# Optimization experiments

Hardware: AMD Instinct MI355X
Metric: run time of the kernel (lower is better)

The kernel has to match this reference:

```python
import jax, jax.numpy as jnp
import numpy as np

N = 10000      # nodes
E = 160000     # edges
F_IN = 84
H = 256
P = 4          # powers [0,1,2,3]
L = 3          # mixhop layers


def setup_inputs() -> dict:
    key = jax.random.key(0)
    ks = jax.random.split(key, 10)
    s = 0.05
    inp = {}
    inp["x"] = jax.random.normal(ks[0], (N, F_IN), jnp.float32)
    inp["edge_index"] = jax.random.randint(ks[1], (2, E), 0, N, dtype=jnp.int32)
    inp["w_in"] = jax.random.normal(ks[2], (F_IN, H), jnp.float32) * s
    inp["b_in"] = jnp.zeros((H,), jnp.float32)
    inp["mh_w0"] = jax.random.normal(ks[3], (P, H, H), jnp.float32) * s
    inp["mh_b0"] = jnp.zeros((P, H), jnp.float32)
    inp["mh_w12"] = jax.random.normal(ks[4], (2, P, P * H, H), jnp.float32) * s
    inp["mh_b12"] = jnp.zeros((2, P, H), jnp.float32)
    inp["ln_g"] = jnp.ones((L, P * H), jnp.float32)
    inp["ln_b"] = jnp.zeros((L, P * H), jnp.float32)
    inp["w1"] = jax.random.normal(ks[5], (P * H, H), jnp.float32) * s
    inp["b1"] = jnp.zeros((H,), jnp.float32)
    inp["w2"] = jax.random.normal(ks[6], (H, H // 2), jnp.float32) * s
    inp["b2"] = jnp.zeros((H // 2,), jnp.float32)
    inp["w3"] = jax.random.normal(ks[7], (H // 2, 1), jnp.float32) * s
    inp["b3"] = jnp.zeros((1,), jnp.float32)
    return inp


def _gcn_norm(edge_index, n):
    # D^{-1/2} (A + I) D^{-1/2}, PyG gcn_norm with add_self_loops=True
    loop = jnp.arange(n, dtype=edge_index.dtype)
    src = jnp.concatenate([edge_index[0], loop])
    dst = jnp.concatenate([edge_index[1], loop])
    deg = jax.ops.segment_sum(jnp.ones(src.shape[0], jnp.float32), dst, num_segments=n)
    dinv = jnp.where(deg > 0, deg ** -0.5, 0.0)
    return src, dst, dinv[src] * dinv[dst]


def _propagate(h, src, dst, w, n):
    # out[i] = sum_{(j->i)} w_e * h[j]
    return jax.ops.segment_sum(h[src] * w[:, None], dst, num_segments=n)


def _mixhop(h, src, dst, w, n, W, B):
    outs = [h @ W[0] + B[0]]  # power 0
    for p in range(1, W.shape[0]):
        h = _propagate(h, src, dst, w, n)
        outs.append(h @ W[p] + B[p])
    return jnp.concatenate(outs, axis=-1)  # [n, P*H]


def _layernorm(x, g, b, eps=1e-5):
    mu = x.mean(-1, keepdims=True)
    var = x.var(-1, keepdims=True)
    return (x - mu) * jax.lax.rsqrt(var + eps) * g + b


def reference(x, edge_index, w_in, b_in, mh_w0, mh_b0, mh_w12, mh_b12,
              ln_g, ln_b, w1, b1, w2, b2, w3, b3):
    gelu = lambda t: jax.nn.gelu(t, approximate=False)  # torch default (erf)
    n = x.shape[0]
    src, dst, w = _gcn_norm(edge_index, n)
    h = gelu(x @ w_in + b_in)
    for i in range(L):
        W, B = (mh_w0, mh_b0) if i == 0 else (mh_w12[i - 1], mh_b12[i - 1])
        h = _mixhop(h, src, dst, w, n, W, B)
        h = gelu(_layernorm(h, ln_g[i], ln_b[i]))
        # dropout inactive at inference
    h = gelu(h @ w1 + b1)
    h = gelu(h @ w2 + b2)
    out = h @ w3 + b3
    return out.squeeze(-1)  # [N]
```

## Files before the change

### kernel.cpp

```cpp
#include <hip/hip_runtime.h>

typedef unsigned short u16;
typedef unsigned char u8;
typedef unsigned int u32;
typedef __bf16 bf16x8 __attribute__((ext_vector_type(8)));
typedef float f32x4 __attribute__((ext_vector_type(4)));
typedef float f32x2 __attribute__((ext_vector_type(2)));

#define NN 10000
#define EE 160000
#define MPAD 10112

__device__ inline float b2f(u16 u) { return __uint_as_float(((u32)u) << 16); }
__device__ inline u16 f2b(float f) {
    u32 u = __float_as_uint(f);
    return (u16)((u + 0x7fffu + ((u >> 16) & 1u)) >> 16);
}
__device__ inline u8 f2f8(float v) {
    return (u8)(__builtin_amdgcn_cvt_pk_fp8_f32(v, v, 0, false) & 0xff);
}
__device__ inline float gelu_f(float x) {
    return 0.5f * x * (1.0f + erff(x * 0.70710678118654752f));
}
__device__ inline void load_lds16(const u16* g, u16* l) {
    __builtin_amdgcn_global_load_lds((const __attribute__((address_space(1))) u32*)g,
                                     (__attribute__((address_space(3))) u32*)l, 16, 0, 0);
}

__global__ __launch_bounds__(256) void k_scan(const int* __restrict__ cnt, int* __restrict__ rowptr,
                                              int* __restrict__ cursor, float* __restrict__ dinv) {
    __shared__ int part[256];
    const int t = threadIdx.x;
    const int CH = 40;
    int base = t * CH;
    int ssum = 0;
    for (int k = 0; k < CH; k++) { int i = base + k; if (i < NN) ssum += cnt[i]; }
    part[t] = ssum;
    __syncthreads();
    for (int off = 1; off < 256; off <<= 1) {
        int v = (t >= off) ? part[t - off] : 0;
        __syncthreads();
        part[t] += v;
        __syncthreads();
    }
    int run = part[t] - ssum;
    for (int k = 0; k < CH; k++) {
        int i = base + k;
        if (i < NN) {
            rowptr[i] = run; cursor[i] = run;
            int c = cnt[i];
            dinv[i] = rsqrtf((float)(c + 1));
            run += c;
        }
    }
    if (t == 255) rowptr[NN] = run;
}

__global__ __launch_bounds__(256) void k_fill(const int* __restrict__ src, const int* __restrict__ dst,
                                              int* __restrict__ cursor, int* __restrict__ cols,
                                              float* __restrict__ vals, const float* __restrict__ dinv) {
    int e = blockIdx.x * 256 + threadIdx.x;
    if (e < EE) {
        int s = src[e], d = dst[e];
        int pos = atomicAdd(&cursor[d], 1);
        cols[pos] = s;
        vals[pos] = dinv[s] * dinv[d];
    }
}

struct TT { const float* src; u16* dst; int K, Nc, Kp; };
struct CvtSrcs { const float *b_in, *mh_b0, *mh_b12, *ln_g, *ln_b, *b1, *b2, *w3, *b3; };
__global__ __launch_bounds__(256) void k_ingest(TT t0, TT t1, TT t2, TT t3, TT t4,
                                                const float* __restrict__ x, u16* __restrict__ xp,
                                                CvtSrcs S, u16* __restrict__ smallC,
                                                const int* __restrict__ dstA, int* __restrict__ cnt) {
    int b = blockIdx.x;
    const int t = threadIdx.x;
    if (b < 656) {
        TT T;
        if (b < 8)        { T = t0; }
        else if (b < 72)  { T = t1; b -= 8; }
        else if (b < 584) { T = t2; b -= 72; }
        else if (b < 648) { T = t3; b -= 584; }
        else              { T = t4; b -= 648; }
        int tk = (T.Kp + 63) >> 6, tn = T.Nc >> 6;
        int bb  = b / (tk * tn);
        int rem = b - bb * (tk * tn);
        int k0 = (rem / tn) * 64, n0 = (rem % tn) * 64;
        __shared__ u16 tile[64][65];
        const float* src = T.src + (size_t)bb * T.K * T.Nc;
        u16* dst = T.dst + (size_t)bb * T.Nc * T.Kp;
        int c = t & 63, r0 = t >> 6;
#pragma unroll
        for (int i = 0; i < 16; i++) {
            int r = r0 + i * 4;
            int k = k0 + r;
            u16 v = 0;
            if (k < T.K) v = f2b(src[(size_t)k * T.Nc + n0 + c]);
            tile[r][c] = v;
        }
        __syncthreads();
        int rr = t & 63, cc0 = t >> 6;
#pragma unroll
        for (int i = 0; i < 16; i++) {
            int cc = cc0 + i * 4;
            int k = k0 + rr;
            if (k < T.Kp) dst[(size_t)(n0 + cc) * T.Kp + k] = tile[rr][cc];
        }
    } else if (b < 5712) {
        int idx = (b - 656) * 256 + t;
        int r = idx >> 7, c = idx & 127;
        u16 v = 0;
        if (r < NN && c < 84) v = f2b(x[(size_t)r * 84 + c]);
        xp[idx] = v;
    } else if (b < 5752) {
        int i = (b - 5712) * 256 + t;
        const float* s; int base;
        if (i < 256)       { s = S.b_in;   base = 0; }
        else if (i < 1280) { s = S.mh_b0;  base = 256; }
        else if (i < 3328) { s = S.mh_b12; base = 1280; }
        else if (i < 6400) { s = S.ln_g;   base = 3328; }
        else if (i < 9472) { s = S.ln_b;   base = 6400; }
        else if (i < 9728) { s = S.b1;     base = 9472; }
        else if (i < 9856) { s = S.b2;     base = 9728; }
        else if (i < 9984) { s = S.w3;     base = 9856; }
        else if (i < 9985) { s = S.b3;     base = 9984; }
        else return;
        smallC[i] = f2b(s[i - base]);
    } else {
        int e = (b - 5752) * 256 + t;
        if (e < EE) atomicAdd(&cnt[dstA[e]], 1);
    }
}

template<int TM, int TN, int ACT, int EPI, int BATCH>
__global__ __launch_bounds__(256) void k_gemm(const u16* __restrict__ A0, const u16* __restrict__ A1,
                                              const u16* __restrict__ A2, const u16* __restrict__ A3,
                                              const u16* __restrict__ Bt, const u16* __restrict__ bias,
                                              u16* __restrict__ C, u8* __restrict__ Z,
                                              const u16* __restrict__ w3c, const u16* __restrict__ b3c,
                                              float* __restrict__ fout,
                                              int K, int ldc, int col0, int NB_M, int NB_N) {
    constexpr int AM = TM / 32, AN = TN / 32;
    constexpr int CA = TM / 16, CB = TN / 16;
    constexpr int NCH = (CA + CB) / 4;
    constexpr int SLOT = (TM + TN) * 32;
    __shared__ __align__(16) u16 Sh[4][SLOT];
    __shared__ float shred[2][64];
    int id = blockIdx.x;
    int g8 = id & 7, sIdx = id >> 3;
    int nb = sIdx % NB_N, jb = sIdx / NB_N;
    int mb = g8 + 8 * jb;
    if (mb >= NB_M) return;
    const u16* A = A0;
    if (BATCH) {
        int z = blockIdx.y;
        if (z == 1) A = A1; else if (z == 2) A = A2; else if (z == 3) A = A3;
        Bt   += (size_t)z * 256 * K;
        bias += z * 256;
        col0 += z * 256;
    }
    const int t = threadIdx.x;
    const int wv = t >> 6, lane = t & 63;
    const int wm = wv >> 1, wn = wv & 1;
    const int quad = lane >> 4, l16 = lane & 15;
    const int tileM = mb * TM, tileN = nb * TN;

    f32x4 acc[AM][AN] = {};

    const int rch = lane >> 2, c8 = (lane & 3) * 8;
    const u16* gsrc[NCH];
    int lofs[NCH];
#pragma unroll
    for (int i = 0; i < NCH; i++) {
        int c = wv + 4 * i;
        if (c < CA) {
            gsrc[i] = A + (size_t)(tileM + c * 16 + rch) * K + c8;
            lofs[i] = c * 512 + lane * 8;
        } else {
            int cc = c - CA;
            gsrc[i] = Bt + (size_t)(tileN + cc * 16 + rch) * K + c8;
            lofs[i] = TM * 32 + cc * 512 + lane * 8;
        }
    }

#pragma unroll
    for (int i = 0; i < NCH; i++) load_lds16(gsrc[i], &Sh[0][lofs[i]]);
#pragma unroll
    for (int i = 0; i < NCH; i++) load_lds16(gsrc[i] + 32, &Sh[1][lofs[i]]);

    const int npair = K >> 6;
    for (int p = 0; p < npair; p++) {
        __syncthreads();
        int cur = (p & 1) << 1;
        int nxt = cur ^ 2;
        int kc = p << 6;
        if (kc + 64 < K) {
#pragma unroll
            for (int i = 0; i < NCH; i++) load_lds16(gsrc[i] + kc + 64, &Sh[nxt][lofs[i]]);
#pragma unroll
            for (int i = 0; i < NCH; i++) load_lds16(gsrc[i] + kc + 96, &Sh[nxt + 1][lofs[i]]);
        }
#pragma unroll
        for (int h = 0; h < 2; h++) {
            const u16* Sb = Sh[cur + h];
            bf16x8 af[AM], bfr[AN];
#pragma unroll
            for (int tm = 0; tm < AM; tm++)
                af[tm] = *(const bf16x8*)&Sb[(wm * (TM / 2) + tm * 16 + l16) * 32 + quad * 8];
#pragma unroll
            for (int tn = 0; tn < AN; tn++)
                bfr[tn] = *(const bf16x8*)&Sb[TM * 32 + (wn * (TN / 2) + tn * 16 + l16) * 32 + quad * 8];
#pragma unroll
            for (int tm = 0; tm < AM; tm++)
#pragma unroll
                for (int tn = 0; tn < AN; tn++)
                    acc[tm][tn] = __builtin_amdgcn_mfma_f32_16x16x32_bf16(af[tm], bfr[tn], acc[tm][tn], 0, 0, 0);
        }
    }

    if (EPI == 3) {
#pragma unroll
        for (int tm = 0; tm < AM; tm++)
#pragma unroll
            for (int r = 0; r < 4; r++) {
                float psum = 0.f;
#pragma unroll
                for (int tn = 0; tn < AN; tn++) {
                    int col = wn * (TN / 2) + tn * 16 + l16;
                    float v = gelu_f(acc[tm][tn][r] + b2f(bias[col]));
                    psum += v * b2f(w3c[col]);
                }
                for (int off = 8; off; off >>= 1) psum += __shfl_down(psum, off);
                if (l16 == 0) shred[wn][wm * (TM / 2) + tm * 16 + quad * 4 + r] = psum;
            }
        __syncthreads();
        if (t < TM) {
            int row = tileM + t;
            if (row < NN) fout[row] = shred[0][t] + shred[1][t] + b2f(b3c[0]);
        }
        return;
    }

#pragma unroll
    for (int tm = 0; tm < AM; tm++)
#pragma unroll
        for (int tn = 0; tn < AN; tn++)
#pragma unroll
            for (int r = 0; r < 4; r++) {
                int row = tileM + wm * (TM / 2) + tm * 16 + quad * 4 + r;
                int col = tileN + wn * (TN / 2) + tn * 16 + l16;
                float v = acc[tm][tn][r];
                if (EPI == 2) {
                    if (col < 256) C[(size_t)row * 1024 + col] = f2b(v + b2f(bias[col]));
                    else           Z[(size_t)row * 768 + (col - 256)] = f2f8(v);
                } else {
                    v += b2f(bias[col]);
                    if (ACT) v = gelu_f(v);
                    C[(size_t)row * ldc + col0 + col] = f2b(v);
                }
            }
}

__global__ __launch_bounds__(256) void k_propw(const u16* __restrict__ hin, int W, int G,
                                               const int* __restrict__ rowptr, const int* __restrict__ cols,
                                               const float* __restrict__ vals, const float* __restrict__ dinv,
                                               u16* __restrict__ out2) {
    int unit = blockIdx.x * 4 + (threadIdx.x >> 6);
    if (unit >= NN * G) return;
    int g = unit / NN, node = unit - g * NN;
    int lane = threadIdx.x & 63;
    int half = lane >> 5, fl = lane & 31;
    const u16* base = hin + g * 256 + fl * 8;
    float a0 = 0, a1 = 0, a2 = 0, a3 = 0, a4 = 0, a5 = 0, a6 = 0, a7 = 0;
    if (half == 1) {
        float di = dinv[node], sw = di * di;
        bf16x8 sv = *(const bf16x8*)(base + (size_t)node * W);
        a0 = sw * (float)sv[0]; a1 = sw * (float)sv[1]; a2 = sw * (float)sv[2]; a3 = sw * (float)sv[3];
        a4 = sw * (float)sv[4]; a5 = sw * (float)sv[5]; a6 = sw * (float)sv[6]; a7 = sw * (float)sv[7];
    }
    int s = rowptr[node], e = rowptr[node + 1];
    int q = s + half;
    for (; q + 6 < e; q += 8) {
        int j0 = cols[q], j1 = cols[q + 2], j2 = cols[q + 4], j3 = cols[q + 6];
        float w0 = vals[q], w1 = vals[q + 2], w2 = vals[q + 4], w3 = vals[q + 6];
        bf16x8 v0 = *(const bf16x8*)(base + (size_t)j0 * W);
        bf16x8 v1 = *(const bf16x8*)(base + (size_t)j1 * W);
        bf16x8 v2 = *(const bf16x8*)(base + (size_t)j2 * W);
        bf16x8 v3 = *(const bf16x8*)(base + (size_t)j3 * W);
        a0 += w0 * (float)v0[0] + w1 * (float)v1[0] + w2 * (float)v2[0] + w3 * (float)v3[0];
        a1 += w0 * (float)v0[1] + w1 * (float)v1[1] + w2 * (float)v2[1] + w3 * (float)v3[1];
        a2 += w0 * (float)v0[2] + w1 * (float)v1[2] + w2 * (float)v2[2] + w3 * (float)v3[2];
        a3 += w0 * (float)v0[3] + w1 * (float)v1[3] + w2 * (float)v2[3] + w3 * (float)v3[3];
        a4 += w0 * (float)v0[4] + w1 * (float)v1[4] + w2 * (float)v2[4] + w3 * (float)v3[4];
        a5 += w0 * (float)v0[5] + w1 * (float)v1[5] + w2 * (float)v2[5] + w3 * (float)v3[5];
        a6 += w0 * (float)v0[6] + w1 * (float)v1[6] + w2 * (float)v2[6] + w3 * (float)v3[6];
        a7 += w0 * (float)v0[7] + w1 * (float)v1[7] + w2 * (float)v2[7] + w3 * (float)v3[7];
    }
    for (; q < e; q += 2) {
        int j = cols[q];
        float w = vals[q];
        bf16x8 v = *(const bf16x8*)(base + (size_t)j * W);
        a0 += w * (float)v[0]; a1 += w * (float)v[1]; a2 += w * (float)v[2]; a3 += w * (float)v[3];
        a4 += w * (float)v[4]; a5 += w * (float)v[5]; a6 += w * (float)v[6]; a7 += w * (float)v[7];
    }
    a0 += __shfl_down(a0, 32); a1 += __shfl_down(a1, 32);
    a2 += __shfl_down(a2, 32); a3 += __shfl_down(a3, 32);
    a4 += __shfl_down(a4, 32); a5 += __shfl_down(a5, 32);
    a6 += __shfl_down(a6, 32); a7 += __shfl_down(a7, 32);
    if (half == 0) {
        int f = fl * 8;
        union { u16 u[8]; uint4 v; } pk;
        pk.u[0] = f2b(a0); pk.u[1] = f2b(a1); pk.u[2] = f2b(a2); pk.u[3] = f2b(a3);
        pk.u[4] = f2b(a4); pk.u[5] = f2b(a5); pk.u[6] = f2b(a6); pk.u[7] = f2b(a7);
        *(uint4*)(out2 + (size_t)node * (size_t)(G * 256) + g * 256 + f) = pk.v;
    }
}

__device__ inline void f8acc(uint2 u, float w, float* a) {
    f32x2 p0 = __builtin_amdgcn_cvt_pk_f32_fp8(u.x, false);
    f32x2 p1 = __builtin_amdgcn_cvt_pk_f32_fp8(u.x, true);
    f32x2 p2 = __builtin_amdgcn_cvt_pk_f32_fp8(u.y, false);
    f32x2 p3 = __builtin_amdgcn_cvt_pk_f32_fp8(u.y, true);
    a[0] += w * p0.x; a[1] += w * p0.y; a[2] += w * p1.x; a[3] += w * p1.y;
    a[4] += w * p2.x; a[5] += w * p2.y; a[6] += w * p3.x; a[7] += w * p3.y;
}
__global__ __launch_bounds__(256) void k_propf8(const u8* __restrict__ hin, int W, int G,
                                                const int* __restrict__ rowptr, const int* __restrict__ cols,
                                                const float* __restrict__ vals, const float* __restrict__ dinv,
                                                u16* __restrict__ concat, const u16* __restrict__ bias,
                                                int col0, u8* __restrict__ out2) {
    int unit = blockIdx.x * 4 + (threadIdx.x >> 6);
    if (unit >= NN * G) return;
    int g = unit / NN, node = unit - g * NN;
    int lane = threadIdx.x & 63;
    int half = lane >> 5, fl = lane & 31;
    const u8* base = hin + g * 256 + fl * 8;
    float a[8] = {0, 0, 0, 0, 0, 0, 0, 0};
    if (half == 1) {
        float di = dinv[node];
        uint2 sv = *(const uint2*)(base + (size_t)node * W);
        f8acc(sv, di * di, a);
    }
    int s = rowptr[node], e = rowptr[node + 1];
    int q = s + half;
    for (; q + 6 < e; q += 8) {
        int j0 = cols[q], j1 = cols[q + 2], j2 = cols[q + 4], j3 = cols[q + 6];
        float w0 = vals[q], w1 = vals[q + 2], w2 = vals[q + 4], w3 = vals[q + 6];
        uint2 v0 = *(const uint2*)(base + (size_t)j0 * W);
        uint2 v1 = *(const uint2*)(base + (size_t)j1 * W);
        uint2 v2 = *(const uint2*)(base + (size_t)j2 * W);
        uint2 v3 = *(const uint2*)(base + (size_t)j3 * W);
        f8acc(v0, w0, a); f8acc(v1, w1, a); f8acc(v2, w2, a); f8acc(v3, w3, a);
    }
    for (; q < e; q += 2) {
        uint2 v = *(const uint2*)(base + (size_t)cols[q] * W);
        f8acc(v, vals[q], a);
    }
#pragma unroll
    for (int i = 0; i < 8; i++) a[i] += __shfl_down(a[i], 32);
    if (half == 0) {
        int f = fl * 8;
        if (g == 0) {
            union { u16 u[8]; uint4 v; } pk;
#pragma unroll
            for (int i = 0; i < 8; i++) pk.u[i] = f2b(a[i] + b2f(bias[f + i]));
            *(uint4*)(concat + (size_t)node * 1024 + col0 + f) = pk.v;
        } else {
            int W2 = W - 256;
            u32 lo = __builtin_amdgcn_cvt_pk_fp8_f32(a[0], a[1], 0, false);
            lo = __builtin_amdgcn_cvt_pk_fp8_f32(a[2], a[3], lo, true);
            u32 hi = __builtin_amdgcn_cvt_pk_fp8_f32(a[4], a[5], 0, false);
            hi = __builtin_amdgcn_cvt_pk_fp8_f32(a[6], a[7], hi, true);
            uint2 o; o.x = lo; o.y = hi;
            *(uint2*)(out2 + (size_t)node * W2 + (g - 1) * 256 + f) = o;
        }
    }
}

__global__ __launch_bounds__(256) void k_ln_gelu(const u16* __restrict__ X, const u16* __restrict__ g,
                                                 const u16* __restrict__ b, u16* __restrict__ out) {
    __shared__ float red[256];
    const int row = blockIdx.x, t = threadIdx.x;
    ushort4 xv = *(const ushort4*)(X + (size_t)row * 1024 + t * 4);
    float x0 = b2f(xv.x), x1 = b2f(xv.y), x2 = b2f(xv.z), x3 = b2f(xv.w);
    red[t] = x0 + x1 + x2 + x3;
    __syncthreads();
    for (int off = 128; off; off >>= 1) {
        if (t < off) red[t] += red[t + off];
        __syncthreads();
    }
    float mu = red[0] * (1.f / 1024.f);
    __syncthreads();
    float d0 = x0 - mu, d1 = x1 - mu, d2 = x2 - mu, d3 = x3 - mu;
    red[t] = d0 * d0 + d1 * d1 + d2 * d2 + d3 * d3;
    __syncthreads();
    for (int off = 128; off; off >>= 1) {
        if (t < off) red[t] += red[t + off];
        __syncthreads();
    }
    float rs = rsqrtf(red[0] * (1.f / 1024.f) + 1e-5f);
    int c = t * 4;
    ushort4 gv = *(const ushort4*)(g + c);
    ushort4 bv = *(const ushort4*)(b + c);
    ushort4 o;
    o.x = f2b(gelu_f(d0 * rs * b2f(gv.x) + b2f(bv.x)));
    o.y = f2b(gelu_f(d1 * rs * b2f(gv.y) + b2f(bv.y)));
    o.z = f2b(gelu_f(d2 * rs * b2f(gv.z) + b2f(bv.z)));
    o.w = f2b(gelu_f(d3 * rs * b2f(gv.w) + b2f(bv.w)));
    *(ushort4*)(out + (size_t)row * 1024 + c) = o;
}

extern "C" void kernel_launch(void* const* d_in, const int* in_sizes, int n_in,
                              void* d_out, int out_size, void* d_ws, size_t ws_size,
                              hipStream_t stream) {
    (void)in_sizes; (void)n_in; (void)out_size; (void)ws_size;
    const float* x  = (const float*)d_in[0];
    const int*   ei = (const int*)d_in[1];
    float* out = (float*)d_out;

    char* p = (char*)d_ws;
    auto alloc = [&](size_t bytes) { char* q = p; p += (bytes + 255) & ~(size_t)255; return q; };
    int*   cnt    = (int*)alloc(NN * 4);
    int*   rowptr = (int*)alloc((NN + 1) * 4);
    int*   cursor = (int*)alloc(NN * 4);
    float* dinv   = (float*)alloc(NN * 4);
    int*   cols   = (int*)alloc(EE * 4);
    float* vals   = (float*)alloc(EE * 4);
    u16*   xp     = (u16*)alloc((size_t)MPAD * 128 * 2);
    u16*   wbuf   = (u16*)alloc((size_t)2686976 * 2);
    u16*   smallC = (u16*)alloc(10240 * 2);
    u16*   S1     = (u16*)alloc((size_t)MPAD * 256 * 2);
    u16*   S2     = (u16*)alloc((size_t)MPAD * 256 * 2);
    u16*   S3     = (u16*)alloc((size_t)MPAD * 256 * 2);
    u16*   S4     = (u16*)alloc((size_t)MPAD * 256 * 2);
    u8*    Zb     = (u8*)alloc((size_t)MPAD * 768);
    u8*    Y2     = (u8*)alloc((size_t)MPAD * 512);
    u8*    Y3     = (u8*)alloc((size_t)MPAD * 256);
    u16*   bufA   = (u16*)alloc((size_t)MPAD * 1024 * 2);
    u16*   concat = (u16*)alloc((size_t)MPAD * 1024 * 2);

    u16* winT  = wbuf;
    u16* w0T   = wbuf + 32768;
    u16* w12T  = wbuf + 294912;
    u16* w1T   = wbuf + 2392064;
    u16* w2T   = wbuf + 2654208;
    u16* binC  = smallC;
    u16* mb0C  = smallC + 256;
    u16* mb12C = smallC + 1280;
    u16* lngC  = smallC + 3328;
    u16* lnbC  = smallC + 6400;
    u16* b1C   = smallC + 9472;
    u16* b2C   = smallC + 9728;
    u16* w3C   = smallC + 9856;
    u16* b3C   = smallC + 9984;

    const int* srcA = ei;
    const int* dstA = ei + EE;

    hipMemsetAsync(cnt, 0, NN * 4, stream);

    TT t0{(const float*)d_in[2],  winT, 84,   256, 128};
    TT t1{(const float*)d_in[4],  w0T,  256,  256, 256};
    TT t2{(const float*)d_in[6],  w12T, 1024, 256, 1024};
    TT t3{(const float*)d_in[10], w1T,  1024, 256, 1024};
    TT t4{(const float*)d_in[12], w2T,  256,  128, 256};
    CvtSrcs CS{(const float*)d_in[3], (const float*)d_in[5], (const float*)d_in[7],
               (const float*)d_in[8], (const float*)d_in[9], (const float*)d_in[11],
               (const float*)d_in[13], (const float*)d_in[14], (const float*)d_in[15]};
    k_ingest<<<6377, 256, 0, stream>>>(t0, t1, t2, t3, t4, x, xp, CS, smallC, dstA, cnt);

    k_scan<<<1, 256, 0, stream>>>(cnt, rowptr, cursor, dinv);
    k_fill<<<(EE + 255) / 256, 256, 0, stream>>>(srcA, dstA, cursor, cols, vals, dinv);

    auto gx = [](int nbm, int nbn) { return 8 * ((nbm + 7) / 8) * nbn; };

    k_gemm<128, 64, 1, 0, 0><<<gx(79, 4), 256, 0, stream>>>(xp, xp, xp, xp, winT, binC, S1, nullptr,
                                                            nullptr, nullptr, nullptr, 128, 256, 0, 79, 4);

    k_propw<<<2500, 256, 0, stream>>>(S1, 256, 1, rowptr, cols, vals, dinv, S2);
    k_propw<<<2500, 256, 0, stream>>>(S2, 256, 1, rowptr, cols, vals, dinv, S3);
    k_propw<<<2500, 256, 0, stream>>>(S3, 256, 1, rowptr, cols, vals, dinv, S4);
    k_gemm<128, 64, 0, 0, 1><<<dim3(gx(79, 4), 4), 256, 0, stream>>>(S1, S2, S3, S4, w0T, mb0C, concat, nullptr,
                                                                     nullptr, nullptr, nullptr, 256, 1024, 0, 79, 4);
    k_ln_gelu<<<NN, 256, 0, stream>>>(concat, lngC, lnbC, bufA);

    for (int L = 0; L < 2; L++) {
        const u16* WT = w12T + (size_t)L * 1024 * 1024;
        const u16* BB = mb12C + L * 1024;
        k_gemm<128, 64, 0, 2, 0><<<gx(79, 16), 256, 0, stream>>>(bufA, bufA, bufA, bufA, WT, BB, concat, Zb,
                                                                 nullptr, nullptr, nullptr, 1024, 0, 0, 79, 16);
        k_propf8<<<7500, 256, 0, stream>>>(Zb, 768, 3, rowptr, cols, vals, dinv, concat, BB + 256, 256, Y2);
        k_propf8<<<5000, 256, 0, stream>>>(Y2, 512, 2, rowptr, cols, vals, dinv, concat, BB + 512, 512, Y3);
        k_propf8<<<2500, 256, 0, stream>>>(Y3, 256, 1, rowptr, cols, vals, dinv, concat, BB + 768, 768, nullptr);
        k_ln_gelu<<<NN, 256, 0, stream>>>(concat, lngC + (L + 1) * 1024, lnbC + (L + 1) * 1024, bufA);
    }

    k_gemm<64, 64, 1, 0, 0><<<gx(158, 4), 256, 0, stream>>>(bufA, bufA, bufA, bufA, w1T, b1C, S1, nullptr,
                                                            nullptr, nullptr, nullptr, 1024, 256, 0, 158, 4);
    k_gemm<64, 128, 0, 3, 0><<<gx(158, 1), 256, 0, stream>>>(S1, S1, S1, S1, w2T, b2C, nullptr, nullptr,
                                                             w3C, b3C, out, 256, 0, 0, 158, 1);
}
```

Before: 454.1 us.

## Reorder first MixHop layer to transform-then-propagate with fp8 propagation

The first MixHop layer now follows the same path as the later layers. It first multiplies the input features by all four power weights in one GEMM, writing power 0 as bf16 and powers 1-3 as fp8. The three propagation passes then run on the narrowing fp8 slices, using the identity A^p(hW) = (A^p h)W. This removes the bf16 propagation kernel, its three 256-wide temporaries and the batched GEMM variant. The cost is that first-layer propagated values are now stored in fp8, which lowers precision.

```diff
diff --git a/kernel.cpp b/kernel.cpp
--- a/kernel.cpp
+++ b/kernel.cpp
@@ -133,10 +133,9 @@
     }
 }
 
-template<int TM, int TN, int ACT, int EPI, int BATCH>
-__global__ __launch_bounds__(256) void k_gemm(const u16* __restrict__ A0, const u16* __restrict__ A1,
-                                              const u16* __restrict__ A2, const u16* __restrict__ A3,
-                                              const u16* __restrict__ Bt, const u16* __restrict__ bias,
+template<int TM, int TN, int ACT, int EPI>
+__global__ __launch_bounds__(256) void k_gemm(const u16* __restrict__ A, const u16* __restrict__ Bt,
+                                              const u16* __restrict__ bias,
                                               u16* __restrict__ C, u8* __restrict__ Z,
                                               const u16* __restrict__ w3c, const u16* __restrict__ b3c,
                                               float* __restrict__ fout,
@@ -152,14 +151,6 @@
     int nb = sIdx % NB_N, jb = sIdx / NB_N;
     int mb = g8 + 8 * jb;
     if (mb >= NB_M) return;
-    const u16* A = A0;
-    if (BATCH) {
-        int z = blockIdx.y;
-        if (z == 1) A = A1; else if (z == 2) A = A2; else if (z == 3) A = A3;
-        Bt   += (size_t)z * 256 * K;
-        bias += z * 256;
-        col0 += z * 256;
-    }
     const int t = threadIdx.x;
     const int wv = t >> 6, lane = t & 63;
     const int wm = wv >> 1, wn = wv & 1;
@@ -260,61 +251,6 @@
                     C[(size_t)row * ldc + col0 + col] = f2b(v);
                 }
             }
-}
-
-__global__ __launch_bounds__(256) void k_propw(const u16* __restrict__ hin, int W, int G,
-                                               const int* __restrict__ rowptr, const int* __restrict__ cols,
-                                               const float* __restrict__ vals, const float* __restrict__ dinv,
-                                               u16* __restrict__ out2) {
-    int unit = blockIdx.x * 4 + (threadIdx.x >> 6);
-    if (unit >= NN * G) return;
-    int g = unit / NN, node = unit - g * NN;
-    int lane = threadIdx.x & 63;
-    int half = lane >> 5, fl = lane & 31;
-    const u16* base = hin + g * 256 + fl * 8;
-    float a0 = 0, a1 = 0, a2 = 0, a3 = 0, a4 = 0, a5 = 0, a6 = 0, a7 = 0;
-    if (half == 1) {
-        float di = dinv[node], sw = di * di;
-        bf16x8 sv = *(const bf16x8*)(base + (size_t)node * W);
-        a0 = sw * (float)sv[0]; a1 = sw * (float)sv[1]; a2 = sw * (float)sv[2]; a3 = sw * (float)sv[3];
-        a4 = sw * (float)sv[4]; a5 = sw * (float)sv[5]; a6 = sw * (float)sv[6]; a7 = sw * (float)sv[7];
-    }
-    int s = rowptr[node], e = rowptr[node + 1];
-    int q = s + half;
-    for (; q + 6 < e; q += 8) {
-        int j0 = cols[q], j1 = cols[q + 2], j2 = cols[q + 4], j3 = cols[q + 6];
-        float w0 = vals[q], w1 = vals[q + 2], w2 = vals[q + 4], w3 = vals[q + 6];
-        bf16x8 v0 = *(const bf16x8*)(base + (size_t)j0 * W);
-        bf16x8 v1 = *(const bf16x8*)(base + (size_t)j1 * W);
-        bf16x8 v2 = *(const bf16x8*)(base + (size_t)j2 * W);
-        bf16x8 v3 = *(const bf16x8*)(base + (size_t)j3 * W);
-        a0 += w0 * (float)v0[0] + w1 * (float)v1[0] + w2 * (float)v2[0] + w3 * (float)v3[0];
-        a1 += w0 * (float)v0[1] + w1 * (float)v1[1] + w2 * (float)v2[1] + w3 * (float)v3[1];
-        a2 += w0 * (float)v0[2] + w1 * (float)v1[2] + w2 * (float)v2[2] + w3 * (float)v3[2];
-        a3 += w0 * (float)v0[3] + w1 * (float)v1[3] + w2 * (float)v2[3] + w3 * (float)v3[3];
-        a4 += w0 * (float)v0[4] + w1 * (float)v1[4] + w2 * (float)v2[4] + w3 * (float)v3[4];
-        a5 += w0 * (float)v0[5] + w1 * (float)v1[5] + w2 * (float)v2[5] + w3 * (float)v3[5];
-        a6 += w0 * (float)v0[6] + w1 * (float)v1[6] + w2 * (float)v2[6] + w3 * (float)v3[6];
-        a7 += w0 * (float)v0[7] + w1 * (float)v1[7] + w2 * (float)v2[7] + w3 * (float)v3[7];
-    }
-    for (; q < e; q += 2) {
-        int j = cols[q];
-        float w = vals[q];
-        bf16x8 v = *(const bf16x8*)(base + (size_t)j * W);
-        a0 += w * (float)v[0]; a1 += w * (float)v[1]; a2 += w * (float)v[2]; a3 += w * (float)v[3];
-        a4 += w * (float)v[4]; a5 += w * (float)v[5]; a6 += w * (float)v[6]; a7 += w * (float)v[7];
-    }
-    a0 += __shfl_down(a0, 32); a1 += __shfl_down(a1, 32);
-    a2 += __shfl_down(a2, 32); a3 += __shfl_down(a3, 32);
-    a4 += __shfl_down(a4, 32); a5 += __shfl_down(a5, 32);
-    a6 += __shfl_down(a6, 32); a7 += __shfl_down(a7, 32);
-    if (half == 0) {
-        int f = fl * 8;
-        union { u16 u[8]; uint4 v; } pk;
-        pk.u[0] = f2b(a0); pk.u[1] = f2b(a1); pk.u[2] = f2b(a2); pk.u[3] = f2b(a3);
-        pk.u[4] = f2b(a4); pk.u[5] = f2b(a5); pk.u[6] = f2b(a6); pk.u[7] = f2b(a7);
-        *(uint4*)(out2 + (size_t)node * (size_t)(G * 256) + g * 256 + f) = pk.v;
-    }
 }
 
 __device__ inline void f8acc(uint2 u, float w, float* a) {
@@ -431,9 +367,6 @@
     u16*   wbuf   = (u16*)alloc((size_t)2686976 * 2);
     u16*   smallC = (u16*)alloc(10240 * 2);
     u16*   S1     = (u16*)alloc((size_t)MPAD * 256 * 2);
-    u16*   S2     = (u16*)alloc((size_t)MPAD * 256 * 2);
-    u16*   S3     = (u16*)alloc((size_t)MPAD * 256 * 2);
-    u16*   S4     = (u16*)alloc((size_t)MPAD * 256 * 2);
     u8*    Zb     = (u8*)alloc((size_t)MPAD * 768);
     u8*    Y2     = (u8*)alloc((size_t)MPAD * 512);
     u8*    Y3     = (u8*)alloc((size_t)MPAD * 256);
@@ -475,29 +408,24 @@
 
     auto gx = [](int nbm, int nbn) { return 8 * ((nbm + 7) / 8) * nbn; };
 
-    k_gemm<128, 64, 1, 0, 0><<<gx(79, 4), 256, 0, stream>>>(xp, xp, xp, xp, winT, binC, S1, nullptr,
-                                                            nullptr, nullptr, nullptr, 128, 256, 0, 79, 4);
-
-    k_propw<<<2500, 256, 0, stream>>>(S1, 256, 1, rowptr, cols, vals, dinv, S2);
-    k_propw<<<2500, 256, 0, stream>>>(S2, 256, 1, rowptr, cols, vals, dinv, S3);
-    k_propw<<<2500, 256, 0, stream>>>(S3, 256, 1, rowptr, cols, vals, dinv, S4);
-    k_gemm<128, 64, 0, 0, 1><<<dim3(gx(79, 4), 4), 256, 0, stream>>>(S1, S2, S3, S4, w0T, mb0C, concat, nullptr,
-                                                                     nullptr, nullptr, nullptr, 256, 1024, 0, 79, 4);
-    k_ln_gelu<<<NN, 256, 0, stream>>>(concat, lngC, lnbC, bufA);
-
-    for (int L = 0; L < 2; L++) {
-        const u16* WT = w12T + (size_t)L * 1024 * 1024;
-        const u16* BB = mb12C + L * 1024;
-        k_gemm<128, 64, 0, 2, 0><<<gx(79, 16), 256, 0, stream>>>(bufA, bufA, bufA, bufA, WT, BB, concat, Zb,
-                                                                 nullptr, nullptr, nullptr, 1024, 0, 0, 79, 16);
+    k_gemm<128, 64, 1, 0><<<gx(79, 4), 256, 0, stream>>>(xp, winT, binC, S1, nullptr,
+                                                         nullptr, nullptr, nullptr, 128, 256, 0, 79, 4);
+
+    for (int L = 0; L < 3; L++) {
+        const u16* Ain = (L == 0) ? S1 : bufA;
+        const u16* WT  = (L == 0) ? w0T : (w12T + (size_t)(L - 1) * 1024 * 1024);
+        const u16* BB  = (L == 0) ? mb0C : (mb12C + (L - 1) * 1024);
+        int K = (L == 0) ? 256 : 1024;
+        k_gemm<128, 64, 0, 2><<<gx(79, 16), 256, 0, stream>>>(Ain, WT, BB, concat, Zb,
+                                                              nullptr, nullptr, nullptr, K, 0, 0, 79, 16);
         k_propf8<<<7500, 256, 0, stream>>>(Zb, 768, 3, rowptr, cols, vals, dinv, concat, BB + 256, 256, Y2);
         k_propf8<<<5000, 256, 0, stream>>>(Y2, 512, 2, rowptr, cols, vals, dinv, concat, BB + 512, 512, Y3);
         k_propf8<<<2500, 256, 0, stream>>>(Y3, 256, 1, rowptr, cols, vals, dinv, concat, BB + 768, 768, nullptr);
-        k_ln_gelu<<<NN, 256, 0, stream>>>(concat, lngC + (L + 1) * 1024, lnbC + (L + 1) * 1024, bufA);
-    }
-
-    k_gemm<64, 64, 1, 0, 0><<<gx(158, 4), 256, 0, stream>>>(bufA, bufA, bufA, bufA, w1T, b1C, S1, nullptr,
-                                                            nullptr, nullptr, nullptr, 1024, 256, 0, 158, 4);
-    k_gemm<64, 128, 0, 3, 0><<<gx(158, 1), 256, 0, stream>>>(S1, S1, S1, S1, w2T, b2C, nullptr, nullptr,
-                                                             w3C, b3C, out, 256, 0, 0, 158, 1);
-}
+        k_ln_gelu<<<NN, 256, 0, stream>>>(concat, lngC + L * 1024, lnbC + L * 1024, bufA);
+    }
+
+    k_gemm<64, 64, 1, 0><<<gx(158, 4), 256, 0, stream>>>(bufA, w1T, b1C, S1, nullptr,
+                                                         nullptr, nullptr, nullptr, 1024, 256, 0, 158, 4);
+    k_gemm<64, 128, 0, 3><<<gx(158, 1), 256, 0, stream>>>(S1, w2T, b2C, nullptr, nullptr,
+                                                          w3C, b3C, out, 256, 0, 0, 158, 1);
+}
```

Result: slower. 470.8 us (+3.7%).
